# Performance work log

Measured on AMD Instinct MI355X. Metric: run time of the kernel, lower is better.

Reference implementation:

```python
import jax, jax.numpy as jnp
import numpy as np

NHEADS = 16
DIM = 1024


def setup_inputs() -> dict:
    key = jax.random.key(0)
    k1, k2, k3 = jax.random.split(key, 3)
    B, S, D = 4, 2048, DIM
    x = jax.random.normal(k1, (B, S, D), dtype=jnp.float32)
    W_qkv = jax.random.normal(k2, (D, 3 * D), dtype=jnp.float32) * (1.0 / np.sqrt(D))
    b_qkv = jax.random.normal(k3, (3 * D,), dtype=jnp.float32) * 0.01
    return {"x": x, "W_qkv": W_qkv, "b_qkv": b_qkv}


def reference(x, W_qkv, b_qkv):
    B, S, D = x.shape
    H = NHEADS
    Dh = D // H
    qkv = x @ W_qkv + b_qkv                      # [B, S, 3D]
    q, k, v = jnp.split(qkv, 3, axis=-1)         # each [B, S, D]
    # [B, S, H, Dh] -> [B, H, S, Dh]
    q = q.reshape(B, S, H, Dh).transpose(0, 2, 1, 3)
    k = k.reshape(B, S, H, Dh).transpose(0, 2, 1, 3)
    v = v.reshape(B, S, H, Dh).transpose(0, 2, 1, 3)
    scale = 1.0 / np.sqrt(Dh).astype(np.float32)
    scores = jnp.einsum('bhqd,bhkd->bhqk', q, k) * scale
    attn = jax.nn.softmax(scores, axis=-1)
    out = jnp.einsum('bhqk,bhkd->bhqd', attn, v)  # [B, H, S, Dh]
    # FAITHFUL to original: raw view [B,H,S,Dh] -> [B, S, H*Dh] (no transpose back)
    return out.reshape(B, S, H * Dh)
```

## Files before the change

### kernel.cpp

```cpp
#include <hip/hip_runtime.h>
#include <hip/hip_bf16.h>
#include <stdint.h>

typedef float          f32x4 __attribute__((ext_vector_type(4)));
typedef short          s16x8 __attribute__((ext_vector_type(8)));
typedef short          s16x4 __attribute__((ext_vector_type(4)));
typedef unsigned short u16;
typedef u16            u16x4 __attribute__((ext_vector_type(4)));
typedef u16            u16x8 __attribute__((ext_vector_type(8)));

#define DMODEL 1024
#define NH     16
#define DH     64
#define SEQ    2048
#define BATCH  4
#define NROW   (BATCH*SEQ)
#define N3     (3*DMODEL)

#define KEXP 0.1803368801f

__device__ __forceinline__ u16 f2bf(float f) {
    __hip_bfloat16 h = __float2bfloat16(f);
    u16 u;
    __builtin_memcpy(&u, &h, 2);
    return u;
}

typedef const __attribute__((address_space(1))) void* gas_t;
typedef __attribute__((address_space(3))) void* las_t;
__device__ __forceinline__ void async16(void* lds, const void* g) {
    __builtin_amdgcn_global_load_lds((gas_t)g, (las_t)lds, 16, 0, 0);
}

__device__ __forceinline__ f32x4 mfma16(s16x8 a, s16x8 b, f32x4 c) {
    return __builtin_amdgcn_mfma_f32_16x16x32_bf16(a, b, c, 0, 0, 0);
}

#if !defined(__HIP_DEVICE_COMPILE__)
__device__ __forceinline__ f32x4 mfma16k16(s16x4 a, s16x4 b, f32x4 c) {
    (void)a; (void)b; return c;
}
#elif __has_builtin(__builtin_amdgcn_mfma_f32_16x16x16bf16_1k)
__device__ __forceinline__ f32x4 mfma16k16(s16x4 a, s16x4 b, f32x4 c) {
    return __builtin_amdgcn_mfma_f32_16x16x16bf16_1k(a, b, c, 0, 0, 0);
}
#elif __has_builtin(__builtin_amdgcn_mfma_f32_16x16x16_bf16)
__device__ __forceinline__ f32x4 mfma16k16(s16x4 a, s16x4 b, f32x4 c) {
    return __builtin_amdgcn_mfma_f32_16x16x16_bf16(a, b, c, 0, 0, 0);
}
#else
#error "no 16x16x16 bf16 mfma builtin on device"
#endif

__global__ __launch_bounds__(256)
void cast_x_kernel(const float* __restrict__ in, u16* __restrict__ out, int n8) {
    int i = blockIdx.x * 256 + threadIdx.x;
    if (i >= n8) return;
    const f32x4* p = (const f32x4*)in;
    f32x4 a = p[2*i], b = p[2*i+1];
    u16x8 o;
    o[0]=f2bf(a[0]); o[1]=f2bf(a[1]); o[2]=f2bf(a[2]); o[3]=f2bf(a[3]);
    o[4]=f2bf(b[0]); o[5]=f2bf(b[1]); o[6]=f2bf(b[2]); o[7]=f2bf(b[3]);
    ((u16x8*)out)[i] = o;
}

__global__ __launch_bounds__(256)
void castT_w_kernel(const float* __restrict__ W, u16* __restrict__ Wt) {
    __shared__ u16 T[64][72];
    const int t  = threadIdx.x;
    const int n0 = blockIdx.x * 64;
    const int k0 = blockIdx.y * 64;
    {
        const int c4 = t & 15, rr = t >> 4;
        #pragma unroll
        for (int ri = 0; ri < 4; ++ri) {
            const int r = ri*16 + rr;
            f32x4 v = *(const f32x4*)&W[(size_t)(k0 + r) * N3 + n0 + c4*4];
            #pragma unroll
            for (int e = 0; e < 4; ++e) T[r][c4*4+e] = f2bf(v[e]);
        }
    }
    __syncthreads();
    {
        const int nr = t >> 2, kq = t & 3;
        #pragma unroll
        for (int pp = 0; pp < 2; ++pp) {
            const int kb = kq + pp*4;
            u16x8 o;
            #pragma unroll
            for (int e = 0; e < 8; ++e) o[e] = T[kb*8+e][nr];
            *(u16x8*)&Wt[(size_t)(n0 + nr) * DMODEL + k0 + kb*8] = o;
        }
    }
}

__global__ __launch_bounds__(256)
void qkv_mfma_kernel(const u16* __restrict__ xb, const u16* __restrict__ Wt,
                     const float* __restrict__ bias,
                     u16* __restrict__ Qb, u16* __restrict__ Kb, u16* __restrict__ Vt)
{
    __shared__ u16 As[128*32];
    __shared__ u16 Bs[128*32];

    const int tid  = threadIdx.x;
    const int lane = tid & 63;
    const int w    = tid >> 6;
    const int wm   = w >> 1, wn = w & 1;
    const int n0   = blockIdx.x * 128;
    const int m0   = blockIdx.y * 128;

    const int srow = w*32 + (lane >> 2);
    const int scol = (lane & 3) * 8;
    u16* ad0 = &As[(w*2+0)*512 + lane*8];
    u16* ad1 = &As[(w*2+1)*512 + lane*8];
    u16* bd0 = &Bs[(w*2+0)*512 + lane*8];
    u16* bd1 = &Bs[(w*2+1)*512 + lane*8];
    const u16* ag0 = &xb[(size_t)(m0 + srow)      * DMODEL + scol];
    const u16* ag1 = &xb[(size_t)(m0 + srow + 16) * DMODEL + scol];
    const u16* bg0 = &Wt[(size_t)(n0 + srow)      * DMODEL + scol];
    const u16* bg1 = &Wt[(size_t)(n0 + srow + 16) * DMODEL + scol];

    f32x4 acc[4][4];
    #pragma unroll
    for (int i = 0; i < 4; ++i)
        #pragma unroll
        for (int j = 0; j < 4; ++j)
            acc[i][j] = (f32x4){0.f, 0.f, 0.f, 0.f};

    for (int k0 = 0; k0 < DMODEL; k0 += 32) {
        async16(ad0, ag0 + k0);
        async16(ad1, ag1 + k0);
        async16(bd0, bg0 + k0);
        async16(bd1, bg1 + k0);
        __syncthreads();
        s16x8 af[4], bf[4];
        #pragma unroll
        for (int mi = 0; mi < 4; ++mi)
            af[mi] = *(const s16x8*)&As[(wm*64 + mi*16 + (lane&15))*32 + (lane>>4)*8];
        #pragma unroll
        for (int ni = 0; ni < 4; ++ni)
            bf[ni] = *(const s16x8*)&Bs[(wn*64 + ni*16 + (lane&15))*32 + (lane>>4)*8];
        #pragma unroll
        for (int mi = 0; mi < 4; ++mi)
            #pragma unroll
            for (int ni = 0; ni < 4; ++ni)
                acc[mi][ni] = mfma16(af[mi], bf[ni], acc[mi][ni]);
        __syncthreads();
    }

    const int part  = n0 >> 10;
    const int col_l = lane & 15;
    const int h     = ((n0 & 1023) >> 6) + wn;
    float bv[4];
    #pragma unroll
    for (int ni = 0; ni < 4; ++ni) bv[ni] = bias[n0 + wn*64 + ni*16 + col_l];

    const int rbase = m0 + wm*64 + (lane>>4)*4;
    u16* qk = (part == 0) ? Qb : Kb;
    #pragma unroll
    for (int mi = 0; mi < 4; ++mi) {
        const int r0 = rbase + mi*16;
        const int b  = r0 >> 11;
        const int s  = r0 & 2047;
        #pragma unroll
        for (int ni = 0; ni < 4; ++ni) {
            const int d = ni*16 + col_l;
            if (part < 2) {
                u16* base = &qk[(((size_t)b*NH + h)*SEQ + s)*DH + d];
                #pragma unroll
                for (int j = 0; j < 4; ++j) {
                    float v = acc[mi][ni][j] + bv[ni];
                    if (part == 0) v *= KEXP;
                    base[(size_t)j*DH] = f2bf(v);
                }
            } else {
                u16x4 o;
                #pragma unroll
                for (int j = 0; j < 4; ++j) o[j] = f2bf(acc[mi][ni][j] + bv[ni]);
                *(u16x4*)&Vt[(((size_t)b*NH + h)*DH + d)*SEQ + s] = o;
            }
        }
    }
}

__global__ __launch_bounds__(512)
void attn_mfma_kernel(const u16* __restrict__ Qb, const u16* __restrict__ Kb,
                      const u16* __restrict__ Vt, float* __restrict__ out)
{
    __shared__ u16 Ks[2][64*64];
    __shared__ u16 Vs[2][64*64];

    const int tid  = threadIdx.x;
    const int lane = tid & 63;
    const int w    = tid >> 6;
    const int q0   = blockIdx.x * 256;
    const int bh   = blockIdx.y;
    const size_t qkoff = (size_t)bh * SEQ * DH;

    const int lrow = lane >> 4;
    const int lcol = lane & 15;

    s16x8 qf[2][2];
    #pragma unroll
    for (int mi = 0; mi < 2; ++mi) {
        const u16* qp = &Qb[qkoff + (size_t)(q0 + w*32 + mi*16 + lcol)*DH + lrow*8];
        qf[mi][0] = *(const s16x8*)(qp);
        qf[mi][1] = *(const s16x8*)(qp + 32);
    }

    const int skey = tid >> 3;
    const int sg   = tid & 7;
    const int gsw8 = (sg ^ (skey & 7)) * 8;
    const int sdo  = tid * 8;
    const u16* kgb = &Kb[qkoff + (size_t)skey * DH + gsw8];
    const u16* vgb = &Vt[((size_t)bh * DH + skey) * SEQ + gsw8];

    f32x4 oacc[2][4];
    #pragma unroll
    for (int mi = 0; mi < 2; ++mi)
        #pragma unroll
        for (int nd = 0; nd < 4; ++nd) oacc[mi][nd] = (f32x4){0.f,0.f,0.f,0.f};
    float psum[2] = {0.f, 0.f};

#define STAGE(buf, kb) do {                                       \
        const int _k0 = (kb) * 64;                                \
        async16(&Ks[buf][sdo], kgb + (size_t)_k0*DH);             \
        async16(&Vs[buf][sdo], vgb + _k0);                        \
    } while (0)

#define COMPUTE(buf) do {                                                        \
        const char* ksb = (const char*)Ks[buf];                                  \
        const char* vsb = (const char*)Vs[buf];                                  \
        f32x4 sacc[2][4];                                                        \
        _Pragma("unroll")                                                        \
        for (int mi = 0; mi < 2; ++mi)                                           \
            _Pragma("unroll")                                                    \
            for (int ni = 0; ni < 4; ++ni) sacc[mi][ni] = (f32x4){0.f,0.f,0.f,0.f}; \
        _Pragma("unroll")                                                        \
        for (int ni = 0; ni < 4; ++ni) {                                         \
            const int key  = ni*16 + lcol;                                       \
            const int rowb = key * 128;                                          \
            _Pragma("unroll")                                                    \
            for (int ks = 0; ks < 2; ++ks) {                                     \
                const int cb = (ks*64 + lrow*16) ^ ((key & 7) << 4);             \
                s16x8 kf = *(const s16x8*)(ksb + rowb + cb);                     \
                _Pragma("unroll")                                                \
                for (int mi = 0; mi < 2; ++mi)                                   \
                    sacc[mi][ni] = mfma16(kf, qf[mi][ks], sacc[mi][ni]);         \
            }                                                                    \
        }                                                                        \
                \
        s16x4 pa[2][4];                                                          \
        _Pragma("unroll")                                                        \
        for (int mi = 0; mi < 2; ++mi) {                                         \
            float rs = 0.f;                                                      \
            _Pragma("unroll")                                                    \
            for (int ni = 0; ni < 4; ++ni) {                                     \
                u16x4 pk;                                                        \
                _Pragma("unroll")                                                \
                for (int jj = 0; jj < 4; ++jj) {                                 \
                    const float p = __builtin_amdgcn_exp2f(sacc[mi][ni][jj]);    \
                    rs += p;                                                     \
                    pk[jj] = f2bf(p);                                            \
                }                                                                \
                pa[mi][ni] = (s16x4)pk;                                          \
            }                                                                    \
            psum[mi] += rs;                                                      \
        }                                                                        \
                \
        _Pragma("unroll")                                                        \
        for (int ni = 0; ni < 4; ++ni) {                                         \
            _Pragma("unroll")                                                    \
            for (int nd = 0; nd < 4; ++nd) {                                     \
                const int d    = nd*16 + lcol;                                   \
                const int gran = ni*2 + (lrow >> 1);                             \
                const int vb   = d*128 + ((gran ^ (d & 7)) << 4) + (lrow & 1)*8; \
                s16x4 vf = *(const s16x4*)(vsb + vb);                            \
                _Pragma("unroll")                                                \
                for (int mi = 0; mi < 2; ++mi)                                   \
                    oacc[mi][nd] = mfma16k16(pa[mi][ni], vf, oacc[mi][nd]);      \
            }                                                                    \
        }                                                                        \
    } while (0)

    STAGE(0, 0);
    asm volatile("s_waitcnt vmcnt(0)" ::: "memory");
    __builtin_amdgcn_s_barrier();

    for (int kb = 0; kb < SEQ/64; kb += 2) {
        STAGE(1, kb + 1);
        COMPUTE(0);
        asm volatile("s_waitcnt vmcnt(0)" ::: "memory");
        __builtin_amdgcn_s_barrier();
        if (kb + 2 < SEQ/64) STAGE(0, kb + 2);
        COMPUTE(1);
        asm volatile("s_waitcnt vmcnt(0)" ::: "memory");
        __builtin_amdgcn_s_barrier();
    }

#undef STAGE
#undef COMPUTE

    float* op = out + qkoff;
    #pragma unroll
    for (int mi = 0; mi < 2; ++mi) {
        float l = psum[mi];
        l += __shfl_xor(l, 16);
        l += __shfl_xor(l, 32);
        #pragma unroll
        for (int jj = 0; jj < 4; ++jj) {
            const float rinv = 1.0f / __shfl(l, lrow*4 + jj);
            const int q = q0 + w*32 + mi*16 + lrow*4 + jj;
            #pragma unroll
            for (int nd = 0; nd < 4; ++nd)
                op[(size_t)q*DH + nd*16 + lcol] = oacc[mi][nd][jj] * rinv;
        }
    }
}

extern "C" void kernel_launch(void* const* d_in, const int* in_sizes, int n_in,
                              void* d_out, int out_size, void* d_ws, size_t ws_size,
                              hipStream_t stream)
{
    const float* x    = (const float*)d_in[0];
    const float* W    = (const float*)d_in[1];
    const float* bias = (const float*)d_in[2];
    float* out = (float*)d_out;

    u16* xb = (u16*)d_ws;
    u16* Wt = xb + (size_t)NROW * DMODEL;
    u16* Qb = Wt + (size_t)N3 * DMODEL;
    u16* Kb = Qb + (size_t)BATCH*NH*SEQ*DH;
    u16* Vt = Kb + (size_t)BATCH*NH*SEQ*DH;

    cast_x_kernel<<<4096, 256, 0, stream>>>(x, xb, NROW*DMODEL/8);
    castT_w_kernel<<<dim3(N3/64, DMODEL/64), 256, 0, stream>>>(W, Wt);
    qkv_mfma_kernel<<<dim3(N3/128, NROW/128), 256, 0, stream>>>(xb, Wt, bias, Qb, Kb, Vt);
    attn_mfma_kernel<<<dim3(SEQ/256, BATCH*NH), 512, 0, stream>>>(Qb, Kb, Vt, out);
}
```

Baseline: 182.3 us.

## Fuse x and W cast kernels; double attention KV stage size to 128 keys

Merges the x cast and the W cast-transpose into one launch, using a block-index split to remove one kernel launch. In the attention kernel each pipeline stage now loads 128 keys (two 64-key sub-tiles) instead of 64, halving the number of barriers and waitcnt drains per sequence. This doubles attention shared memory to 64 KB per block, which may lower occupancy.

```diff
diff --git a/kernel.cpp b/kernel.cpp
--- a/kernel.cpp
+++ b/kernel.cpp
@@ -53,23 +53,24 @@
 #endif
 
 __global__ __launch_bounds__(256)
-void cast_x_kernel(const float* __restrict__ in, u16* __restrict__ out, int n8) {
-    int i = blockIdx.x * 256 + threadIdx.x;
-    if (i >= n8) return;
-    const f32x4* p = (const f32x4*)in;
-    f32x4 a = p[2*i], b = p[2*i+1];
-    u16x8 o;
-    o[0]=f2bf(a[0]); o[1]=f2bf(a[1]); o[2]=f2bf(a[2]); o[3]=f2bf(a[3]);
-    o[4]=f2bf(b[0]); o[5]=f2bf(b[1]); o[6]=f2bf(b[2]); o[7]=f2bf(b[3]);
-    ((u16x8*)out)[i] = o;
-}
-
-__global__ __launch_bounds__(256)
-void castT_w_kernel(const float* __restrict__ W, u16* __restrict__ Wt) {
+void cast_fused_kernel(const float* __restrict__ xin, u16* __restrict__ xb,
+                       const float* __restrict__ W,  u16* __restrict__ Wt)
+{
     __shared__ u16 T[64][72];
-    const int t  = threadIdx.x;
-    const int n0 = blockIdx.x * 64;
-    const int k0 = blockIdx.y * 64;
+    const int t = threadIdx.x;
+    if (blockIdx.x < 4096) {
+        const int i = blockIdx.x * 256 + t;
+        const f32x4* p = (const f32x4*)xin;
+        f32x4 a = p[2*i], b = p[2*i+1];
+        u16x8 o;
+        o[0]=f2bf(a[0]); o[1]=f2bf(a[1]); o[2]=f2bf(a[2]); o[3]=f2bf(a[3]);
+        o[4]=f2bf(b[0]); o[5]=f2bf(b[1]); o[6]=f2bf(b[2]); o[7]=f2bf(b[3]);
+        ((u16x8*)xb)[i] = o;
+        return;
+    }
+    const int bid2 = blockIdx.x - 4096;
+    const int n0 = (bid2 % (N3/64)) * 64;
+    const int k0 = (bid2 / (N3/64)) * 64;
     {
         const int c4 = t & 15, rr = t >> 4;
         #pragma unroll
@@ -187,8 +188,8 @@
 void attn_mfma_kernel(const u16* __restrict__ Qb, const u16* __restrict__ Kb,
                       const u16* __restrict__ Vt, float* __restrict__ out)
 {
-    __shared__ u16 Ks[2][64*64];
-    __shared__ u16 Vs[2][64*64];
+    __shared__ u16 Ks[2][2][64*64];
+    __shared__ u16 Vs[2][2][64*64];
 
     const int tid  = threadIdx.x;
     const int lane = tid & 63;
@@ -222,15 +223,17 @@
         for (int nd = 0; nd < 4; ++nd) oacc[mi][nd] = (f32x4){0.f,0.f,0.f,0.f};
     float psum[2] = {0.f, 0.f};
 
-#define STAGE(buf, kb) do {                                       \
-        const int _k0 = (kb) * 64;                                \
-        async16(&Ks[buf][sdo], kgb + (size_t)_k0*DH);             \
-        async16(&Vs[buf][sdo], vgb + _k0);                        \
+#define STAGE(buf, kb2) do {                                          \
+        const size_t _o = (size_t)(kb2) * 128;                        \
+        async16(&Ks[buf][0][sdo], kgb + (_o     ) * DH);              \
+        async16(&Ks[buf][1][sdo], kgb + (_o + 64) * DH);              \
+        async16(&Vs[buf][0][sdo], vgb + _o);                          \
+        async16(&Vs[buf][1][sdo], vgb + _o + 64);                     \
     } while (0)
 
-#define COMPUTE(buf) do {                                                        \
-        const char* ksb = (const char*)Ks[buf];                                  \
-        const char* vsb = (const char*)Vs[buf];                                  \
+#define COMPUTE(buf, sub) do {                                                   \
+        const char* ksb = (const char*)Ks[buf][sub];                             \
+        const char* vsb = (const char*)Vs[buf][sub];                             \
         f32x4 sacc[2][4];                                                        \
         _Pragma("unroll")                                                        \
         for (int mi = 0; mi < 2; ++mi)                                           \
@@ -287,13 +290,15 @@
     asm volatile("s_waitcnt vmcnt(0)" ::: "memory");
     __builtin_amdgcn_s_barrier();
 
-    for (int kb = 0; kb < SEQ/64; kb += 2) {
-        STAGE(1, kb + 1);
-        COMPUTE(0);
+    for (int kb2 = 0; kb2 < SEQ/128; kb2 += 2) {
+        STAGE(1, kb2 + 1);
+        COMPUTE(0, 0);
+        COMPUTE(0, 1);
         asm volatile("s_waitcnt vmcnt(0)" ::: "memory");
         __builtin_amdgcn_s_barrier();
-        if (kb + 2 < SEQ/64) STAGE(0, kb + 2);
-        COMPUTE(1);
+        if (kb2 + 2 < SEQ/128) STAGE(0, kb2 + 2);
+        COMPUTE(1, 0);
+        COMPUTE(1, 1);
         asm volatile("s_waitcnt vmcnt(0)" ::: "memory");
         __builtin_amdgcn_s_barrier();
     }
@@ -333,8 +338,7 @@
     u16* Kb = Qb + (size_t)BATCH*NH*SEQ*DH;
     u16* Vt = Kb + (size_t)BATCH*NH*SEQ*DH;
 
-    cast_x_kernel<<<4096, 256, 0, stream>>>(x, xb, NROW*DMODEL/8);
-    castT_w_kernel<<<dim3(N3/64, DMODEL/64), 256, 0, stream>>>(W, Wt);
+    cast_fused_kernel<<<4096 + 768, 256, 0, stream>>>(x, xb, W, Wt);
     qkv_mfma_kernel<<<dim3(N3/128, NROW/128), 256, 0, stream>>>(xb, Wt, bias, Qb, Kb, Vt);
     attn_mfma_kernel<<<dim3(SEQ/256, BATCH*NH), 512, 0, stream>>>(Qb, Kb, Vt, out);
 }
```

After: 172.7 us. 5.3% less time.
